# Performance work log

Hardware: AMD Instinct MI355X
Metric: run time of the kernel (lower is better)

The kernel has to match this reference:

```python
import jax, jax.numpy as jnp
import numpy as np

DIM = 512
CODEBOOK_SIZE = 8192


def setup_inputs() -> dict:
    key = jax.random.key(0)
    k_x, k_e = jax.random.split(key)
    x = jax.random.normal(k_x, (4, 4096, DIM), dtype=jnp.float32)
    # EuclideanCodebook buffer: embed ~ randn(codebook_size, dim)
    embed = jax.random.normal(k_e, (CODEBOOK_SIZE, DIM), dtype=jnp.float32)
    return {"x": x, "embed": embed}


def reference(x, embed):
    # projection_in / projection_out are Identity (codebook_dim=None)
    shape = x.shape
    flatten = x.reshape(-1, shape[-1])  # [N, D]
    # dist = -(||f||^2 - 2 f @ e^T + ||e||^2)  -> negative squared euclidean
    f_sq = jnp.sum(flatten * flatten, axis=1, keepdims=True)          # [N, 1]
    e_sq = jnp.sum(embed * embed, axis=1)[None, :]                    # [1, K]
    dist = -(f_sq - 2.0 * flatten @ embed.T + e_sq)                   # [N, K]
    embed_ind = jnp.argmax(dist, axis=-1)                             # [N]
    embed_ind = embed_ind.reshape(shape[:-1])                         # [B, S]
    quantize = jnp.take(embed, embed_ind, axis=0)                     # [B, S, D]
    return quantize, embed_ind
```

## Files before the change

### kernel.cpp

```cpp
#include <hip/hip_runtime.h>

#define DIM    512
#define KCODES 8192
#define NROWS  16384
#define NEG_INF -3.402823466e38f
#define MARGIN 1.0f
#define CPR 128

typedef unsigned short ushort_t;
typedef unsigned int uint_t;
typedef __attribute__((ext_vector_type(8))) short v8s;
typedef __attribute__((ext_vector_type(4))) float v4f;

__device__ inline ushort_t f32_to_bf16_rne(float f) {
    uint_t u = __float_as_uint(f);
    uint_t r = u + 0x7fffu + ((u >> 16) & 1u);
    return (ushort_t)(r >> 16);
}

__device__ inline int4 cvt8hi(float4 a, float4 b) {
    ushort_t h[8] = { f32_to_bf16_rne(a.x), f32_to_bf16_rne(a.y),
                      f32_to_bf16_rne(a.z), f32_to_bf16_rne(a.w),
                      f32_to_bf16_rne(b.x), f32_to_bf16_rne(b.y),
                      f32_to_bf16_rne(b.z), f32_to_bf16_rne(b.w) };
    int4 p;
    p.x = (int)((uint_t)h[0] | ((uint_t)h[1] << 16));
    p.y = (int)((uint_t)h[2] | ((uint_t)h[3] << 16));
    p.z = (int)((uint_t)h[4] | ((uint_t)h[5] << 16));
    p.w = (int)((uint_t)h[6] | ((uint_t)h[7] << 16));
    return p;
}

__device__ inline void dma16(const void* g, void* l) {
    __builtin_amdgcn_global_load_lds(
        (const __attribute__((address_space(1))) unsigned int*)g,
        (__attribute__((address_space(3))) unsigned int*)l, 16, 0, 0);
}

__global__ __launch_bounds__(512) void convert_kernel(
    const float* __restrict__ x, const float* __restrict__ embed,
    int4* __restrict__ e_t, int4* __restrict__ x_t,
    float* __restrict__ e_sq, float* __restrict__ esqh,
    float* __restrict__ f_sq)
{
    __shared__ int4 buf[64][65];

    const int w = threadIdx.x >> 6;
    const int lane = threadIdx.x & 63;
    const bool isE = blockIdx.x < (KCODES / 64);
    const int rows0 = isE ? blockIdx.x * 64 : (blockIdx.x - KCODES / 64) * 64;
    const float* src_base = isE ? embed : x;

    #pragma unroll
    for (int rr = 0; rr < 8; ++rr) {
        int r_local = w * 8 + rr;
        const float* src = src_base + (size_t)(rows0 + r_local) * DIM + lane * 8;
        float4 a = *(const float4*)src;
        float4 b = *(const float4*)(src + 4);
        buf[r_local][(lane + 2 * r_local) & 63] = cvt8hi(a, b);
        float s = a.x*a.x + a.y*a.y + a.z*a.z + a.w*a.w
                + b.x*b.x + b.y*b.y + b.z*b.z + b.w*b.w;
        #pragma unroll
        for (int off = 32; off >= 1; off >>= 1) s += __shfl_down(s, off, 64);
        if (lane == 0) {
            int r = rows0 + r_local;
            if (isE) { e_sq[r] = s; esqh[r] = -0.5f * s; }
            else     { f_sq[r] = s; }
        }
    }
    __syncthreads();

    #pragma unroll
    for (int i = 0; i < 8; ++i) {
        int sq = w * 8 + i;
        int4 v = buf[lane][(sq + 2 * lane) & 63];
        if (isE) e_t[(size_t)sq * KCODES + rows0 + lane] = v;
        else     x_t[(size_t)sq * NROWS  + rows0 + lane] = v;
    }
}

__global__ __launch_bounds__(512, 2) void screen_kernel(
    const int4* __restrict__ e_t, const int4* __restrict__ x_t,
    const float* __restrict__ esqh,
    float* __restrict__ cand_s, int* __restrict__ cand_i)
{
    __shared__ __align__(16) short EH[2][8][256][8];
    __shared__ __align__(16) short XH[2][8][256][8];

    const int t = threadIdx.x;
    const int w = t >> 6;
    const int lane = t & 63;
    const int quad = lane >> 4;
    const int l15 = lane & 15;
    const int wm = w & 1;
    const int wn = w >> 1;

    const int n = blockIdx.x;
    const int xcd = n & 7;
    const int j = n >> 3;
    const int rt = xcd * 8 + (j & 7);
    const int ct = j >> 3;
    const int row0 = rt * 256;
    const int cbase = ct * 256;

    const bool isE = w < 4;
    const int4* gbase = isE ? (e_t + cbase + w * 64 + lane)
                            : (x_t + row0 + (w - 4) * 64 + lane);
    const size_t gstride = isE ? KCODES : NROWS;

    v4f acc[8][4];
    #pragma unroll
    for (int mi = 0; mi < 8; ++mi) {
        float4 sd = *(const float4*)(esqh + cbase + wm * 128 + mi * 16 + quad * 4);
        v4f sv = (v4f){sd.x, sd.y, sd.z, sd.w};
        #pragma unroll
        for (int nj = 0; nj < 4; ++nj) acc[mi][nj] = sv;
    }

    auto issue_dma = [&](int S) {
        int buf = S & 1;
        short* ldst = isE ? &EH[buf][0][(w & 3) * 64][0] : &XH[buf][0][(w & 3) * 64][0];
        #pragma unroll
        for (int q = 0; q < 8; ++q) {
            int sq = S * 8 + q;
            dma16(gbase + (size_t)sq * gstride, ldst + q * 256 * 8);
        }
    };

    issue_dma(0);

    for (int S = 0; S < 8; ++S) {
        __syncthreads();
        if (S < 7) issue_dma(S + 1);
        const int buf = S & 1;

        #pragma unroll
        for (int ks = 0; ks < 2; ++ks) {
            const int q = ks * 4 + quad;
            v8s bh[4];
            #pragma unroll
            for (int nj = 0; nj < 4; ++nj)
                bh[nj] = *(const v8s*)(&XH[buf][q][wn * 64 + nj * 16 + l15][0]);
            #pragma unroll
            for (int mi = 0; mi < 8; ++mi) {
                v8s ah = *(const v8s*)(&EH[buf][q][wm * 128 + mi * 16 + l15][0]);
                #pragma unroll
                for (int nj = 0; nj < 4; ++nj)
                    acc[mi][nj] = __builtin_amdgcn_mfma_f32_16x16x32_bf16(ah, bh[nj], acc[mi][nj], 0, 0, 0);
            }
        }
    }

    #pragma unroll
    for (int nj = 0; nj < 4; ++nj) {
        float b1 = NEG_INF, b2 = NEG_INF;
        int   i1 = 0, i2 = 0;
        #pragma unroll
        for (int g = 0; g < 4; ++g) {
            v4f s0 = acc[2 * g][nj], s1 = acc[2 * g + 1][nj];
            float m = fmaxf(fmaxf(fmaxf(s0[0], s0[1]), fmaxf(s0[2], s0[3])),
                            fmaxf(fmaxf(s1[0], s1[1]), fmaxf(s1[2], s1[3])));
            int gid = cbase + wm * 128 + g * 32 + quad * 4;
            if (m > b1)      { b2 = b1; i2 = i1; b1 = m; i1 = gid; }
            else if (m > b2) { b2 = m;  i2 = gid; }
        }
        #pragma unroll
        for (int o = 16; o <= 32; o <<= 1) {
            float c1 = __shfl_xor(b1, o, 64);
            int   j1 = __shfl_xor(i1, o, 64);
            float c2 = __shfl_xor(b2, o, 64);
            int   j2 = __shfl_xor(i2, o, 64);
            if (c1 > b1) {
                b2 = fmaxf(b1, c2); i2 = (b1 >= c2) ? i1 : j2;
                b1 = c1; i1 = j1;
            } else {
                i2 = (b2 >= c1) ? i2 : j1;
                b2 = fmaxf(b2, c1);
            }
        }
        if (quad == 0) {
            int row = row0 + wn * 64 + nj * 16 + l15;
            size_t b = (size_t)row * CPR + (ct * 4 + wm * 2);
            cand_s[b]     = b1;  cand_i[b]     = i1;
            cand_s[b + 1] = b2;  cand_i[b + 1] = i2;
        }
    }
}

__global__ __launch_bounds__(256) void rescore_kernel(
    const float* __restrict__ x, const float* __restrict__ embed,
    const float* __restrict__ e_sq, const float* __restrict__ f_sq,
    const float* __restrict__ cand_s, const int* __restrict__ cand_i,
    float* __restrict__ out)
{
    int row = blockIdx.x * 4 + (threadIdx.x >> 6);
    int lane = threadIdx.x & 63;
    size_t cb = (size_t)row * CPR;

    float cs0 = cand_s[cb + lane];
    float cs1 = cand_s[cb + 64 + lane];
    int   ci0 = cand_i[cb + lane];
    int   ci1 = cand_i[cb + 64 + lane];

    float m = fmaxf(cs0, cs1);
    #pragma unroll
    for (int o = 32; o >= 1; o >>= 1) m = fmaxf(m, __shfl_xor(m, o, 64));

    unsigned long long mask0 = __ballot(cs0 >= m - MARGIN);
    unsigned long long mask1 = __ballot(cs1 >= m - MARGIN);

    const float4* xsrc = (const float4*)(x + (size_t)row * DIM + lane * 8);
    float4 xa = xsrc[0], xb = xsrc[1];
    float fsq = f_sq[row];

    float bd = NEG_INF;
    int   bi = 0x7fffffff;

    #pragma unroll
    for (int s = 0; s < 2; ++s) {
        unsigned long long mask = s ? mask1 : mask0;
        while (mask) {
            int p = __ffsll(mask) - 1;
            mask &= mask - 1;
            int base = __shfl(s ? ci1 : ci0, p);
            float4 EA[8], EB[8];
            #pragma unroll
            for (int e8 = 0; e8 < 8; ++e8) {
                int c = base + ((e8 >> 2) << 4) + (e8 & 3);
                const float4* er = (const float4*)(embed + (size_t)c * DIM + lane * 8);
                EA[e8] = er[0]; EB[e8] = er[1];
            }
            #pragma unroll
            for (int e8 = 0; e8 < 8; ++e8) {
                int c = base + ((e8 >> 2) << 4) + (e8 & 3);
                float part = xa.x*EA[e8].x + xa.y*EA[e8].y + xa.z*EA[e8].z + xa.w*EA[e8].w
                           + xb.x*EB[e8].x + xb.y*EB[e8].y + xb.z*EB[e8].z + xb.w*EB[e8].w;
                #pragma unroll
                for (int o = 32; o >= 1; o >>= 1) part += __shfl_xor(part, o, 64);
                float d = -((fsq - 2.0f * part) + e_sq[c]);
                if (d > bd || (d == bd && c < bi)) { bd = d; bi = c; }
            }
        }
    }

    const float4* er = (const float4*)(embed + (size_t)bi * DIM + lane * 8);
    float4 qa = er[0], qb = er[1];
    float4* dst = (float4*)(out + (size_t)row * DIM + lane * 8);
    dst[0] = qa; dst[1] = qb;
    if (lane == 0) out[(size_t)NROWS * DIM + row] = (float)bi;
}

extern "C" void kernel_launch(void* const* d_in, const int* in_sizes, int n_in,
                              void* d_out, int out_size, void* d_ws, size_t ws_size,
                              hipStream_t stream)
{
    const float* x     = (const float*)d_in[0];
    const float* embed = (const float*)d_in[1];
    float* out = (float*)d_out;

    float* e_sq   = (float*)d_ws;
    float* esqh   = e_sq + KCODES;
    float* f_sq   = esqh + KCODES;
    float* cand_s = f_sq + NROWS;
    int*   cand_i = (int*)(cand_s + (size_t)NROWS * CPR);
    int4*  e_t    = (int4*)(cand_i + (size_t)NROWS * CPR);

    int4* x_t = (int4*)d_out;

    (void)in_sizes; (void)n_in; (void)out_size; (void)ws_size;

    convert_kernel<<<(KCODES + NROWS) / 64, 512, 0, stream>>>(
        x, embed, e_t, x_t, e_sq, esqh, f_sq);
    screen_kernel<<<2048, 512, 0, stream>>>(
        e_t, x_t, esqh, cand_s, cand_i);
    rescore_kernel<<<NROWS / 4, 256, 0, stream>>>(
        x, embed, e_sq, f_sq, cand_s, cand_i, out);
}
```

Baseline: 260.8 us.

## Quantize screening GEMM to int8 with per-row scales and i8 MFMA

Replaces the bf16 screening GEMM with symmetric per-row int8 quantization of x and the codebook, using the 16x16x64 i8 MFMA and dequantizing with row scales before the top-2 candidate selection. This halves the bytes staged and moved through LDS and halves the K-loop iterations, which targets the screening kernel's memory and MFMA throughput. The coarser approximation is offset by widening the rescore margin from 1 to 4, which may admit more candidates into the exact fp32 rescoring pass. The conversion kernel now also computes a per-row absmax and stores the scale arrays.

```diff
diff --git a/kernel.cpp b/kernel.cpp
--- a/kernel.cpp
+++ b/kernel.cpp
@@ -4,32 +4,13 @@
 #define KCODES 8192
 #define NROWS  16384
 #define NEG_INF -3.402823466e38f
-#define MARGIN 1.0f
+#define MARGIN 4.0f
 #define CPR 128
 
 typedef unsigned short ushort_t;
 typedef unsigned int uint_t;
-typedef __attribute__((ext_vector_type(8))) short v8s;
+typedef __attribute__((ext_vector_type(4))) int   v4i;
 typedef __attribute__((ext_vector_type(4))) float v4f;
-
-__device__ inline ushort_t f32_to_bf16_rne(float f) {
-    uint_t u = __float_as_uint(f);
-    uint_t r = u + 0x7fffu + ((u >> 16) & 1u);
-    return (ushort_t)(r >> 16);
-}
-
-__device__ inline int4 cvt8hi(float4 a, float4 b) {
-    ushort_t h[8] = { f32_to_bf16_rne(a.x), f32_to_bf16_rne(a.y),
-                      f32_to_bf16_rne(a.z), f32_to_bf16_rne(a.w),
-                      f32_to_bf16_rne(b.x), f32_to_bf16_rne(b.y),
-                      f32_to_bf16_rne(b.z), f32_to_bf16_rne(b.w) };
-    int4 p;
-    p.x = (int)((uint_t)h[0] | ((uint_t)h[1] << 16));
-    p.y = (int)((uint_t)h[2] | ((uint_t)h[3] << 16));
-    p.z = (int)((uint_t)h[4] | ((uint_t)h[5] << 16));
-    p.w = (int)((uint_t)h[6] | ((uint_t)h[7] << 16));
-    return p;
-}
 
 __device__ inline void dma16(const void* g, void* l) {
     __builtin_amdgcn_global_load_lds(
@@ -39,11 +20,12 @@
 
 __global__ __launch_bounds__(512) void convert_kernel(
     const float* __restrict__ x, const float* __restrict__ embed,
-    int4* __restrict__ e_t, int4* __restrict__ x_t,
+    int4* __restrict__ e_t8, int4* __restrict__ x_t8,
     float* __restrict__ e_sq, float* __restrict__ esqh,
-    float* __restrict__ f_sq)
-{
-    __shared__ int4 buf[64][65];
+    float* __restrict__ f_sq,
+    float* __restrict__ e_scale, float* __restrict__ f_scale)
+{
+    __shared__ __align__(16) char buf[64][528];
 
     const int w = threadIdx.x >> 6;
     const int lane = threadIdx.x & 63;
@@ -57,35 +39,53 @@
         const float* src = src_base + (size_t)(rows0 + r_local) * DIM + lane * 8;
         float4 a = *(const float4*)src;
         float4 b = *(const float4*)(src + 4);
-        buf[r_local][(lane + 2 * r_local) & 63] = cvt8hi(a, b);
         float s = a.x*a.x + a.y*a.y + a.z*a.z + a.w*a.w
                 + b.x*b.x + b.y*b.y + b.z*b.z + b.w*b.w;
-        #pragma unroll
-        for (int off = 32; off >= 1; off >>= 1) s += __shfl_down(s, off, 64);
+        float am = fmaxf(fmaxf(fmaxf(fabsf(a.x), fabsf(a.y)), fmaxf(fabsf(a.z), fabsf(a.w))),
+                         fmaxf(fmaxf(fabsf(b.x), fabsf(b.y)), fmaxf(fabsf(b.z), fabsf(b.w))));
+        #pragma unroll
+        for (int off = 32; off >= 1; off >>= 1) {
+            s += __shfl_xor(s, off, 64);
+            am = fmaxf(am, __shfl_xor(am, off, 64));
+        }
+        float inv = (am > 0.0f) ? 127.0f / am : 0.0f;
+
+        float vq[8] = {a.x, a.y, a.z, a.w, b.x, b.y, b.z, b.w};
+        uint_t lo = 0, hi = 0;
+        #pragma unroll
+        for (int jj = 0; jj < 4; ++jj) {
+            lo |= ((uint_t)((int)rintf(vq[jj]     * inv) & 0xff)) << (8 * jj);
+            hi |= ((uint_t)((int)rintf(vq[4 + jj] * inv) & 0xff)) << (8 * jj);
+        }
+        *(int*)&buf[r_local][8 * lane]     = (int)lo;
+        *(int*)&buf[r_local][8 * lane + 4] = (int)hi;
+
         if (lane == 0) {
             int r = rows0 + r_local;
-            if (isE) { e_sq[r] = s; esqh[r] = -0.5f * s; }
-            else     { f_sq[r] = s; }
+            float sc = am * (1.0f / 127.0f);
+            if (isE) { e_sq[r] = s; esqh[r] = -0.5f * s; e_scale[r] = sc; }
+            else     { f_sq[r] = s; f_scale[r] = sc; }
         }
     }
     __syncthreads();
 
     #pragma unroll
-    for (int i = 0; i < 8; ++i) {
-        int sq = w * 8 + i;
-        int4 v = buf[lane][(sq + 2 * lane) & 63];
-        if (isE) e_t[(size_t)sq * KCODES + rows0 + lane] = v;
-        else     x_t[(size_t)sq * NROWS  + rows0 + lane] = v;
+    for (int i = 0; i < 4; ++i) {
+        int sq = w * 4 + i;
+        int4 v = *(const int4*)&buf[lane][16 * sq];
+        if (isE) e_t8[(size_t)sq * KCODES + rows0 + lane] = v;
+        else     x_t8[(size_t)sq * NROWS  + rows0 + lane] = v;
     }
 }
 
 __global__ __launch_bounds__(512, 2) void screen_kernel(
-    const int4* __restrict__ e_t, const int4* __restrict__ x_t,
+    const int4* __restrict__ e_t8, const int4* __restrict__ x_t8,
     const float* __restrict__ esqh,
+    const float* __restrict__ e_scale, const float* __restrict__ f_scale,
     float* __restrict__ cand_s, int* __restrict__ cand_i)
 {
-    __shared__ __align__(16) short EH[2][8][256][8];
-    __shared__ __align__(16) short XH[2][8][256][8];
+    __shared__ __align__(16) char EH[2][8][256][16];
+    __shared__ __align__(16) char XH[2][8][256][16];
 
     const int t = threadIdx.x;
     const int w = t >> 6;
@@ -104,62 +104,75 @@
     const int cbase = ct * 256;
 
     const bool isE = w < 4;
-    const int4* gbase = isE ? (e_t + cbase + w * 64 + lane)
-                            : (x_t + row0 + (w - 4) * 64 + lane);
+    const int4* gbase = isE ? (e_t8 + cbase + w * 64 + lane)
+                            : (x_t8 + row0 + (w - 4) * 64 + lane);
     const size_t gstride = isE ? KCODES : NROWS;
 
-    v4f acc[8][4];
-    #pragma unroll
-    for (int mi = 0; mi < 8; ++mi) {
-        float4 sd = *(const float4*)(esqh + cbase + wm * 128 + mi * 16 + quad * 4);
-        v4f sv = (v4f){sd.x, sd.y, sd.z, sd.w};
-        #pragma unroll
-        for (int nj = 0; nj < 4; ++nj) acc[mi][nj] = sv;
-    }
+    v4i acc[8][4];
+    #pragma unroll
+    for (int mi = 0; mi < 8; ++mi)
+        #pragma unroll
+        for (int nj = 0; nj < 4; ++nj)
+            acc[mi][nj] = (v4i){0, 0, 0, 0};
 
     auto issue_dma = [&](int S) {
         int buf = S & 1;
-        short* ldst = isE ? &EH[buf][0][(w & 3) * 64][0] : &XH[buf][0][(w & 3) * 64][0];
+        char* ldst = isE ? &EH[buf][0][(w & 3) * 64][0] : &XH[buf][0][(w & 3) * 64][0];
         #pragma unroll
         for (int q = 0; q < 8; ++q) {
             int sq = S * 8 + q;
-            dma16(gbase + (size_t)sq * gstride, ldst + q * 256 * 8);
+            dma16(gbase + (size_t)sq * gstride, ldst + q * 256 * 16);
         }
     };
 
     issue_dma(0);
 
-    for (int S = 0; S < 8; ++S) {
+    for (int S = 0; S < 4; ++S) {
         __syncthreads();
-        if (S < 7) issue_dma(S + 1);
+        if (S < 3) issue_dma(S + 1);
         const int buf = S & 1;
 
         #pragma unroll
         for (int ks = 0; ks < 2; ++ks) {
             const int q = ks * 4 + quad;
-            v8s bh[4];
+            v4i bh[4];
             #pragma unroll
             for (int nj = 0; nj < 4; ++nj)
-                bh[nj] = *(const v8s*)(&XH[buf][q][wn * 64 + nj * 16 + l15][0]);
+                bh[nj] = *(const v4i*)(&XH[buf][q][wn * 64 + nj * 16 + l15][0]);
             #pragma unroll
             for (int mi = 0; mi < 8; ++mi) {
-                v8s ah = *(const v8s*)(&EH[buf][q][wm * 128 + mi * 16 + l15][0]);
+                v4i ah = *(const v4i*)(&EH[buf][q][wm * 128 + mi * 16 + l15][0]);
                 #pragma unroll
                 for (int nj = 0; nj < 4; ++nj)
-                    acc[mi][nj] = __builtin_amdgcn_mfma_f32_16x16x32_bf16(ah, bh[nj], acc[mi][nj], 0, 0, 0);
-            }
-        }
+                    acc[mi][nj] = __builtin_amdgcn_mfma_i32_16x16x64_i8(ah, bh[nj], acc[mi][nj], 0, 0, 0);
+            }
+        }
+    }
+
+    v4f se4[8], eq4[8];
+    #pragma unroll
+    for (int mi = 0; mi < 8; ++mi) {
+        se4[mi] = *(const v4f*)(e_scale + cbase + wm * 128 + mi * 16 + quad * 4);
+        eq4[mi] = *(const v4f*)(esqh    + cbase + wm * 128 + mi * 16 + quad * 4);
     }
 
     #pragma unroll
     for (int nj = 0; nj < 4; ++nj) {
+        float sfv = f_scale[row0 + wn * 64 + nj * 16 + l15];
         float b1 = NEG_INF, b2 = NEG_INF;
         int   i1 = 0, i2 = 0;
         #pragma unroll
         for (int g = 0; g < 4; ++g) {
-            v4f s0 = acc[2 * g][nj], s1 = acc[2 * g + 1][nj];
-            float m = fmaxf(fmaxf(fmaxf(s0[0], s0[1]), fmaxf(s0[2], s0[3])),
-                            fmaxf(fmaxf(s1[0], s1[1]), fmaxf(s1[2], s1[3])));
+            float m = NEG_INF;
+            #pragma unroll
+            for (int h = 0; h < 2; ++h) {
+                int mi = 2 * g + h;
+                #pragma unroll
+                for (int jj = 0; jj < 4; ++jj) {
+                    float sc = fmaf(sfv * se4[mi][jj], (float)acc[mi][nj][jj], eq4[mi][jj]);
+                    m = fmaxf(m, sc);
+                }
+            }
             int gid = cbase + wm * 128 + g * 32 + quad * 4;
             if (m > b1)      { b2 = b1; i2 = i1; b1 = m; i1 = gid; }
             else if (m > b2) { b2 = m;  i2 = gid; }
@@ -258,21 +271,23 @@
     const float* embed = (const float*)d_in[1];
     float* out = (float*)d_out;
 
-    float* e_sq   = (float*)d_ws;
-    float* esqh   = e_sq + KCODES;
-    float* f_sq   = esqh + KCODES;
-    float* cand_s = f_sq + NROWS;
-    int*   cand_i = (int*)(cand_s + (size_t)NROWS * CPR);
-    int4*  e_t    = (int4*)(cand_i + (size_t)NROWS * CPR);
-
-    int4* x_t = (int4*)d_out;
+    float* e_sq    = (float*)d_ws;
+    float* esqh    = e_sq + KCODES;
+    float* f_sq    = esqh + KCODES;
+    float* e_scale = f_sq + NROWS;
+    float* f_scale = e_scale + KCODES;
+    float* cand_s  = f_scale + NROWS;
+    int*   cand_i  = (int*)(cand_s + (size_t)NROWS * CPR);
+    int4*  e_t8    = (int4*)(cand_i + (size_t)NROWS * CPR);
+
+    int4* x_t8 = (int4*)d_out;
 
     (void)in_sizes; (void)n_in; (void)out_size; (void)ws_size;
 
     convert_kernel<<<(KCODES + NROWS) / 64, 512, 0, stream>>>(
-        x, embed, e_t, x_t, e_sq, esqh, f_sq);
+        x, embed, e_t8, x_t8, e_sq, esqh, f_sq, e_scale, f_scale);
     screen_kernel<<<2048, 512, 0, stream>>>(
-        e_t, x_t, esqh, cand_s, cand_i);
+        e_t8, x_t8, esqh, e_scale, f_scale, cand_s, cand_i);
     rescore_kernel<<<NROWS / 4, 256, 0, stream>>>(
         x, embed, e_sq, f_sq, cand_s, cand_i, out);
 }
```

Result: no change. 260.3 us (-0.2%).
